# Kernel tuning notes

Measured on AMD Instinct MI355X. Metric: run time of the kernel, lower is better.

## Reference

```python
import jax, jax.numpy as jnp
import numpy as np

CONF_THRESH = 0.01
TOP_K = 200
NMS_THRESH = 0.45


def setup_inputs() -> dict:
    key = jax.random.key(0)
    k1, k2, k3, k4, k5 = jax.random.split(key, 5)
    B, N, C = 32, 8732, 21
    return {
        "loc_data": jax.random.normal(k1, (B, N, 4), jnp.float32),
        "conf_data": jax.random.normal(k2, (B, N, C), jnp.float32),
        "pose_data": jax.random.normal(k3, (B, N, 32), jnp.float32),
        "line_data": jax.random.normal(k4, (B, N, 3), jnp.float32),
        "dbox_list": jax.random.uniform(k5, (N, 4), jnp.float32),
    }


def decode(loc, dbox):
    # loc, dbox: [N,4]; variances 0.1 / 0.2 as in the torch decode()
    cxcy = dbox[:, :2] + loc[:, :2] * 0.1 * dbox[:, 2:]
    wh = dbox[:, 2:] * jnp.exp(loc[:, 2:] * 0.2)
    mins = cxcy - wh / 2.0
    maxs = mins + wh
    return jnp.concatenate([mins, maxs], axis=1)  # [N,4] xyxy


def nms_class(boxes, scores, poses, lines):
    """Greedy NMS for one (batch, class). boxes [N,4], scores [N] (softmax probs).
    Matches torch nm_suppression: candidates are the top_k by score above
    conf_thresh; suppress IoU > overlap; at most top_k kept."""
    s0 = jnp.where(scores > CONF_THRESH, scores, -jnp.inf)
    _, cand_idx = jax.lax.top_k(s0, TOP_K)  # descending-score candidate pool
    cb = boxes[cand_idx]                     # [K,4]
    cs = s0[cand_idx]                        # [K], -inf where below threshold
    x1, y1, x2, y2 = cb[:, 0], cb[:, 1], cb[:, 2], cb[:, 3]
    area = (x2 - x1) * (y2 - y1)
    K = TOP_K
    ar = jnp.arange(K)

    def step(s, _):
        i = jnp.argmax(s)
        take = jnp.isfinite(s[i])
        xx1 = jnp.maximum(x1, x1[i])
        yy1 = jnp.maximum(y1, y1[i])
        xx2 = jnp.minimum(x2, x2[i])
        yy2 = jnp.minimum(y2, y2[i])
        inter = jnp.clip(xx2 - xx1, 0.0) * jnp.clip(yy2 - yy1, 0.0)
        union = area - inter + area[i]
        iou = inter / union
        supp = (iou > NMS_THRESH) | (ar == i)
        s_new = jnp.where(take & supp, -jnp.inf, s)
        return s_new, (i, take)

    _, (pos, take) = jax.lax.scan(step, cs, None, length=K)
    gi = cand_idx[pos]  # global box indices of kept detections [K]
    row = jnp.concatenate(
        [scores[gi][:, None], boxes[gi], poses[gi], lines[gi]], axis=1
    )  # [K, 1+4+32+3] = [200, 40]
    return row * take[:, None].astype(row.dtype)


def reference(loc_data, conf_data, pose_data, line_data, dbox_list):
    conf = jax.nn.softmax(conf_data, axis=-1)                       # [B,N,C]
    boxes = jax.vmap(decode, in_axes=(0, None))(loc_data, dbox_list)  # [B,N,4]
    per_cls = jax.vmap(nms_class, in_axes=(None, 1, None, None))    # over classes
    per_batch = jax.vmap(per_cls, in_axes=(0, 0, 0, 0))             # over batch
    out = per_batch(boxes, conf, pose_data, line_data)              # [B,C,200,40]
    return out.at[:, 0].set(0.0)  # class 0 (background) is skipped in torch loop
```

## Files before the change

### kernel.cpp

```cpp
#include <hip/hip_runtime.h>
#include <math.h>

#define BB 32
#define NN 8732
#define CC 21
#define TOPK 200
#define NPOSE 32
#define NLINE 3
#define NBINS 2048
#define CAP 1024
#define ROWW 40

__device__ __forceinline__ double fexp(double x) {
  const double LOG2E = 1.4426950408889634074;
  const double LN2HI = 6.93147180369123816490e-01;
  const double LN2LO = 1.90821492927058770002e-10;
  double kd = rint(x * LOG2E);
  double r = fma(-kd, LN2HI, x);
  r = fma(-kd, LN2LO, r);
  double p = 2.08767569878680989792e-09;
  p = fma(p, r, 2.50521083854417187751e-08);
  p = fma(p, r, 2.75573192239858906526e-07);
  p = fma(p, r, 2.75573192239858925110e-06);
  p = fma(p, r, 2.48015873015873015873e-05);
  p = fma(p, r, 1.98412698412698412698e-04);
  p = fma(p, r, 1.38888888888888888889e-03);
  p = fma(p, r, 8.33333333333333333333e-03);
  p = fma(p, r, 4.16666666666666666667e-02);
  p = fma(p, r, 1.66666666666666666667e-01);
  p = fma(p, r, 0.5);
  p = fma(p, r, 1.0);
  p = fma(p, r, 1.0);
  int k = (int)kd;
  k = k < -1020 ? -1020 : (k > 1020 ? 1020 : k);
  double sc = __longlong_as_double((long long)(1023 + k) << 52);
  return p * sc;
}

__global__ __launch_bounds__(256, 4) void score_kernel(
    const float* __restrict__ conf, float* __restrict__ scores) {
  __shared__ __align__(16) float buf[256 * CC];
  const int tid = threadIdx.x;
  const int i0 = blockIdx.x * 256;
  const int base = i0 * CC;
  int total = BB * NN * CC - base;
  if (total > 256 * CC) total = 256 * CC;
  {
    const float4* g4 = (const float4*)(conf + base);
    float4* b4 = (float4*)buf;
    const int n4 = total >> 2;
    for (int t = tid; t < n4; t += 256) b4[t] = g4[t];
  }
  __syncthreads();
  const int i = i0 + tid;
  if (i >= BB * NN) return;
  const float* p = buf + tid * CC;
  float x[CC];
#pragma unroll
  for (int c = 0; c < CC; ++c) x[c] = p[c];
  float m = x[0];
#pragma unroll
  for (int c = 1; c < CC; ++c) m = fmaxf(m, x[c]);
  float e[CC];
#pragma unroll
  for (int c = 0; c < CC; ++c) e[c] = (float)fexp((double)(x[c] - m));
  float r0 = e[0] + e[8], r1 = e[1] + e[9], r2 = e[2] + e[10], r3 = e[3] + e[11];
  float r4 = e[4] + e[12], r5 = e[5] + e[13], r6 = e[6] + e[14], r7 = e[7] + e[15];
  float sum = ((r0 + r1) + (r2 + r3)) + ((r4 + r5) + (r6 + r7));
  sum += e[16]; sum += e[17]; sum += e[18]; sum += e[19]; sum += e[20];
  const int b = i / NN, n = i - b * NN;
#pragma unroll
  for (int c = 0; c < CC; ++c)
    scores[((size_t)b * CC + c) * NN + n] = e[c] / sum;
}

__device__ __forceinline__ int score_bin(float s) {
  unsigned u = __float_as_uint(s);
  int bin = (int)(u >> 15) - 30720;
  return bin < 0 ? 0 : (bin > NBINS - 1 ? NBINS - 1 : bin);
}

__device__ __forceinline__ float score_full(const float* conf, int b, int c, int n) {
  const float* p = conf + ((size_t)b * NN + n) * CC;
  float mm = p[0];
  for (int c2 = 1; c2 < CC; ++c2) mm = fmaxf(mm, p[c2]);
  float e[CC];
  for (int c2 = 0; c2 < CC; ++c2) e[c2] = (float)fexp((double)(p[c2] - mm));
  float r0 = e[0] + e[8], r1 = e[1] + e[9], r2 = e[2] + e[10], r3 = e[3] + e[11];
  float r4 = e[4] + e[12], r5 = e[5] + e[13], r6 = e[6] + e[14], r7 = e[7] + e[15];
  float sum = ((r0 + r1) + (r2 + r3)) + ((r4 + r5) + (r6 + r7));
  sum += e[16]; sum += e[17]; sum += e[18]; sum += e[19]; sum += e[20];
  return e[c] / sum;
}

__global__ __launch_bounds__(256) void nms_kernel(
    const float* __restrict__ loc, const float* __restrict__ conf,
    const float* __restrict__ pose, const float* __restrict__ line,
    const float* __restrict__ dbox, const float* __restrict__ scores,
    int mode, float* __restrict__ out) {
  const int bc = blockIdx.x;
  const int b = bc / CC, c = bc - b * CC;
  const int tid = threadIdx.x;
  const int wv = tid >> 6, lane = tid & 63;
  float* outSlab = out + (size_t)bc * (TOPK * ROWW);
  const float4 z4 = make_float4(0.f, 0.f, 0.f, 0.f);

  if (c == 0) {
    float4* o4 = (float4*)outSlab;
    for (int i = tid; i < TOPK * ROWW / 4; i += 256) o4[i] = z4;
    return;
  }

  __shared__ int hist[NBINS];
  __shared__ unsigned long long ckey[CAP];
  __shared__ float4 cbox[TOPK];
  __shared__ float carea[TOPK];
  __shared__ float sScore[TOPK];
  __shared__ int sIdx[TOPK];
  __shared__ unsigned long long supp[TOPK * 4];
  __shared__ unsigned long long rowAnyBits[4];
  __shared__ int kept[TOPK];
  __shared__ int waveTot[4];
  __shared__ int sBT, sCnt, sKept;

  for (int i = tid; i < NBINS; i += 256) hist[i] = 0;
  if (tid == 0) { sCnt = 0; sBT = 0; }
  __syncthreads();

  const float* scoresB = scores + ((size_t)b * CC + c) * NN;

  float4 v[9];
  if (mode == 1) {
#pragma unroll
    for (int k = 0; k < 8; ++k)
      v[k] = *(const float4*)(scoresB + k * 1024 + tid * 4);
    if (tid < 135)
      v[8] = *(const float4*)(scoresB + 8192 + tid * 4);
    else
      v[8] = make_float4(-1.f, -1.f, -1.f, -1.f);
  } else {
#pragma unroll 1
    for (int k = 0; k < 9; ++k) {
      const int n0 = k * 1024 + (tid << 2);
      if (k < 8 || tid < 135) {
        v[k].x = score_full(conf, b, c, n0 + 0);
        v[k].y = score_full(conf, b, c, n0 + 1);
        v[k].z = score_full(conf, b, c, n0 + 2);
        v[k].w = score_full(conf, b, c, n0 + 3);
      } else {
        v[k] = make_float4(-1.f, -1.f, -1.f, -1.f);
      }
    }
  }

#pragma unroll
  for (int k = 0; k < 9; ++k) {
    if (v[k].x > 0.01f) atomicAdd(&hist[score_bin(v[k].x)], 1);
    if (v[k].y > 0.01f) atomicAdd(&hist[score_bin(v[k].y)], 1);
    if (v[k].z > 0.01f) atomicAdd(&hist[score_bin(v[k].z)], 1);
    if (v[k].w > 0.01f) atomicAdd(&hist[score_bin(v[k].w)], 1);
  }
  __syncthreads();

  int s8 = 0;
#pragma unroll
  for (int k = 0; k < 8; ++k) s8 += hist[tid * 8 + k];
  int cs = s8;
#pragma unroll
  for (int d = 1; d < 64; d <<= 1) {
    int t = __shfl_down(cs, d, 64);
    if (lane + d < 64) cs += t;
  }
  if (lane == 0) waveTot[wv] = cs;
  __syncthreads();
  {
    int higher = 0;
    for (int g = wv + 1; g < 4; ++g) higher += waveTot[g];
    int incl = cs + higher;
    int excl = incl - s8;
    if (excl < TOPK && incl >= TOPK) {
      int cum = excl, bt = tid * 8;
      for (int bin = tid * 8 + 7;; --bin) {
        cum += hist[bin];
        if (cum >= TOPK || bin == tid * 8) { bt = bin; break; }
      }
      sBT = bt;
    }
  }
  __syncthreads();
  const int bt = sBT;

#pragma unroll
  for (int k = 0; k < 9; ++k) {
    float sv[4] = {v[k].x, v[k].y, v[k].z, v[k].w};
#pragma unroll
    for (int j = 0; j < 4; ++j) {
      float s = sv[j];
      if (s > 0.01f && score_bin(s) >= bt) {
        int p = atomicAdd(&sCnt, 1);
        if (p < CAP) {
          unsigned n = (unsigned)(k * 1024 + (tid << 2) + j);
          ckey[p] = ((unsigned long long)__float_as_uint(s) << 32) |
                    (unsigned long long)(0xFFFFFFFFu - n);
        }
      }
    }
  }
  __syncthreads();
  const int M = sCnt < CAP ? sCnt : CAP;
  if (M == 0) {
    float4* o4 = (float4*)outSlab;
    for (int i = tid; i < TOPK * ROWW / 4; i += 256) o4[i] = z4;
    return;
  }
  const int K = M < TOPK ? M : TOPK;

  for (int t = tid; t < M; t += 256) {
    unsigned long long kt = ckey[t];
    int r = 0;
    for (int j = 0; j < M; ++j) r += (ckey[j] > kt) ? 1 : 0;
    if (r < TOPK) {
      sScore[r] = __uint_as_float((unsigned)(kt >> 32));
      sIdx[r] = (int)(0xFFFFFFFFu - (unsigned)(kt & 0xFFFFFFFFull));
    }
  }
  __syncthreads();

  const float* locB = loc + (size_t)b * NN * 4;
  if (tid < K) {
    int n = sIdx[tid];
    float4 l4 = *(const float4*)(locB + (size_t)n * 4);
    float4 d4 = *(const float4*)(dbox + (size_t)n * 4);
    float cx = d4.x + (l4.x * 0.1f) * d4.z;
    float cy = d4.y + (l4.y * 0.1f) * d4.w;
    float w = d4.z * (float)fexp((double)(l4.z * 0.2f));
    float h = d4.w * (float)fexp((double)(l4.w * 0.2f));
    float x1 = cx - w * 0.5f;
    float y1 = cy - h * 0.5f;
    float x2 = x1 + w;
    float y2 = y1 + h;
    cbox[tid] = make_float4(x1, y1, x2, y2);
    carea[tid] = (x2 - x1) * (y2 - y1);
  }
  __syncthreads();

  {
    const double TMID = (double)0.45f + 0x1p-26;
    const int l = wv * 64 + lane;
    const bool lvalid = l < K;
    float4 lb = lvalid ? cbox[l] : z4;
    float lar = lvalid ? carea[l] : 0.f;
    const int jlim = (K < wv * 64 + 63) ? K : (wv * 64 + 63);
    for (int j = 0; j < jlim; ++j) {
      float4 jb = cbox[j];
      float ja = carea[j];
      float xx1 = fmaxf(lb.x, jb.x);
      float yy1 = fmaxf(lb.y, jb.y);
      float xx2 = fminf(lb.z, jb.z);
      float yy2 = fminf(lb.w, jb.w);
      float iw = fmaxf(xx2 - xx1, 0.0f);
      float ih = fmaxf(yy2 - yy1, 0.0f);
      float inter = iw * ih;
      float uni = (lar - inter) + ja;
      double tt = fma(-TMID, (double)uni, (double)inter);
      bool hit = lvalid & (l > j) & (tt > 0.0);
      unsigned long long mres = __ballot((int)hit);
      if (lane == 0) supp[j * 4 + wv] = mres;
    }
    if (lane == 0)
      for (int j = jlim; j < K; ++j) supp[j * 4 + wv] = 0ull;
  }
  __syncthreads();

  {
    bool nz = false;
    if (tid < K)
      nz = (supp[tid * 4 + 0] | supp[tid * 4 + 1] |
            supp[tid * 4 + 2] | supp[tid * 4 + 3]) != 0ull;
    unsigned long long bal = __ballot((int)nz);
    if (lane == 0) rowAnyBits[wv] = bal;
  }
  __syncthreads();

  if (tid == 0) {
    unsigned long long alive[4];
#pragma unroll
    for (int w = 0; w < 4; ++w) {
      int cnt = K - w * 64;
      alive[w] = cnt <= 0 ? 0ull : (cnt >= 64 ? ~0ull : ((1ull << cnt) - 1ull));
    }
    int nk = 0;
#pragma unroll
    for (int w = 0; w < 4; ++w) {
      const unsigned long long raw = rowAnyBits[w];
      while (alive[w]) {
        int bit = __ffsll(alive[w]) - 1;
        int j = w * 64 + bit;
        kept[nk++] = j;
        alive[w] &= ~(1ull << bit);
        if ((raw >> bit) & 1) {
          unsigned long long r0 = supp[j * 4 + 0];
          unsigned long long r1 = supp[j * 4 + 1];
          unsigned long long r2 = supp[j * 4 + 2];
          unsigned long long r3 = supp[j * 4 + 3];
          alive[0] &= ~r0; alive[1] &= ~r1; alive[2] &= ~r2; alive[3] &= ~r3;
        }
      }
    }
    sKept = nk;
  }
  __syncthreads();

  const int nk = sKept;
  const float* poseB = pose + (size_t)b * NN * NPOSE;
  const float* lineB = line + (size_t)b * NN * NLINE;
  for (int t = tid; t < nk; t += 256) {
    int j = kept[t];
    int n = sIdx[j];
    float* row = outSlab + (size_t)t * ROWW;
    float4 bx = cbox[j];
    row[0] = sScore[j];
    row[1] = bx.x;
    row[2] = bx.y;
    row[3] = bx.z;
    row[4] = bx.w;
    const float4* p4 = (const float4*)(poseB + (size_t)n * NPOSE);
#pragma unroll
    for (int q = 0; q < 8; ++q) {
      float4 pv = p4[q];
      row[5 + 4 * q + 0] = pv.x;
      row[5 + 4 * q + 1] = pv.y;
      row[5 + 4 * q + 2] = pv.z;
      row[5 + 4 * q + 3] = pv.w;
    }
    row[37] = lineB[(size_t)n * NLINE + 0];
    row[38] = lineB[(size_t)n * NLINE + 1];
    row[39] = lineB[(size_t)n * NLINE + 2];
  }
  {
    const int zq = (TOPK - nk) * 10;
    float4* o4 = (float4*)(outSlab + (size_t)nk * ROWW);
    for (int q = tid; q < zq; q += 256) o4[q] = z4;
  }
}

extern "C" void kernel_launch(void* const* d_in, const int* in_sizes, int n_in,
                              void* d_out, int out_size, void* d_ws, size_t ws_size,
                              hipStream_t stream) {
  const float* loc  = (const float*)d_in[0];
  const float* conf = (const float*)d_in[1];
  const float* pose = (const float*)d_in[2];
  const float* line = (const float*)d_in[3];
  const float* dbox = (const float*)d_in[4];
  float* out = (float*)d_out;

  const size_t scoreBytes = (size_t)BB * CC * NN * sizeof(float);
  int mode = (ws_size >= scoreBytes) ? 1 : 0;
  float* scores = mode ? (float*)d_ws : nullptr;

  if (mode) {
    const int total = BB * NN;
    score_kernel<<<(total + 255) / 256, 256, 0, stream>>>(conf, scores);
  }
  nms_kernel<<<BB * CC, 256, 0, stream>>>(loc, conf, pose, line, dbox,
                                          scores, mode, out);
}
```

Baseline: 194.1 us.

## Use table-based exp in softmax and unroll rank-sort and IoU loops

The softmax score kernel replaces a degree-12 double polynomial exp with a 64-entry shared-memory table plus a degree-4 polynomial, which cuts FP64 work per element. The candidate rank sort now reads keys in 16-wide vectorized chunks over a zero-padded array. The IoU suppression-matrix loop is unrolled by 8, batching LDS loads and ballots. The trade-offs are extra shared memory, extra registers, and a small accuracy difference in the exp approximation.

```diff
diff --git a/kernel.cpp b/kernel.cpp
--- a/kernel.cpp
+++ b/kernel.cpp
@@ -11,7 +11,7 @@
 #define CAP 1024
 #define ROWW 40
 
-__device__ __forceinline__ double fexp(double x) {
+__device__ __forceinline__ double fexp12(double x) {
   const double LOG2E = 1.4426950408889634074;
   const double LN2HI = 6.93147180369123816490e-01;
   const double LN2LO = 1.90821492927058770002e-10;
@@ -37,9 +37,30 @@
   return p * sc;
 }
 
+__device__ __forceinline__ double fexp_t(double x, const double* __restrict__ T) {
+  const double INV64 = 1.4426950408889634074 * 64.0;
+  const double L64HI = 6.93147180369123816490e-01 / 64.0;
+  const double L64LO = 1.90821492927058770002e-10 / 64.0;
+  double kd = rint(x * INV64);
+  double r = fma(-kd, L64HI, x);
+  r = fma(-kd, L64LO, r);
+  double p = 4.16666666666666666667e-02;
+  p = fma(p, r, 1.66666666666666666667e-01);
+  p = fma(p, r, 0.5);
+  p = fma(p, r, 1.0);
+  p = fma(p, r, 1.0);
+  int ki = (int)kd;
+  double t = T[ki & 63];
+  int e = ki >> 6;
+  e = e < -1020 ? -1020 : e;
+  double sc = __longlong_as_double((long long)(1023 + e) << 52);
+  return (t * p) * sc;
+}
+
 __global__ __launch_bounds__(256, 4) void score_kernel(
     const float* __restrict__ conf, float* __restrict__ scores) {
   __shared__ __align__(16) float buf[256 * CC];
+  __shared__ double Texp[64];
   const int tid = threadIdx.x;
   const int i0 = blockIdx.x * 256;
   const int base = i0 * CC;
@@ -51,6 +72,8 @@
     const int n4 = total >> 2;
     for (int t = tid; t < n4; t += 256) b4[t] = g4[t];
   }
+  if (tid < 64)
+    Texp[tid] = fexp12((double)tid * (6.93147180369123816490e-01 / 64.0));
   __syncthreads();
   const int i = i0 + tid;
   if (i >= BB * NN) return;
@@ -63,7 +86,7 @@
   for (int c = 1; c < CC; ++c) m = fmaxf(m, x[c]);
   float e[CC];
 #pragma unroll
-  for (int c = 0; c < CC; ++c) e[c] = (float)fexp((double)(x[c] - m));
+  for (int c = 0; c < CC; ++c) e[c] = (float)fexp_t((double)(x[c] - m), Texp);
   float r0 = e[0] + e[8], r1 = e[1] + e[9], r2 = e[2] + e[10], r3 = e[3] + e[11];
   float r4 = e[4] + e[12], r5 = e[5] + e[13], r6 = e[6] + e[14], r7 = e[7] + e[15];
   float sum = ((r0 + r1) + (r2 + r3)) + ((r4 + r5) + (r6 + r7));
@@ -85,7 +108,7 @@
   float mm = p[0];
   for (int c2 = 1; c2 < CC; ++c2) mm = fmaxf(mm, p[c2]);
   float e[CC];
-  for (int c2 = 0; c2 < CC; ++c2) e[c2] = (float)fexp((double)(p[c2] - mm));
+  for (int c2 = 0; c2 < CC; ++c2) e[c2] = (float)fexp12((double)(p[c2] - mm));
   float r0 = e[0] + e[8], r1 = e[1] + e[9], r2 = e[2] + e[10], r3 = e[3] + e[11];
   float r4 = e[4] + e[12], r5 = e[5] + e[13], r6 = e[6] + e[14], r7 = e[7] + e[15];
   float sum = ((r0 + r1) + (r2 + r3)) + ((r4 + r5) + (r6 + r7));
@@ -112,7 +135,7 @@
   }
 
   __shared__ int hist[NBINS];
-  __shared__ unsigned long long ckey[CAP];
+  __shared__ __align__(16) unsigned long long ckey[CAP + 16];
   __shared__ float4 cbox[TOPK];
   __shared__ float carea[TOPK];
   __shared__ float sScore[TOPK];
@@ -214,11 +237,24 @@
     return;
   }
   const int K = M < TOPK ? M : TOPK;
+  const int Mpad = (M + 15) & ~15;
+  for (int i = M + tid; i < Mpad; i += 256) ckey[i] = 0ull;
+  __syncthreads();
 
   for (int t = tid; t < M; t += 256) {
     unsigned long long kt = ckey[t];
     int r = 0;
-    for (int j = 0; j < M; ++j) r += (ckey[j] > kt) ? 1 : 0;
+    for (int j0 = 0; j0 < Mpad; j0 += 16) {
+      ulonglong2 kk[8];
+#pragma unroll
+      for (int q = 0; q < 8; ++q)
+        kk[q] = *(const ulonglong2*)(ckey + j0 + 2 * q);
+#pragma unroll
+      for (int q = 0; q < 8; ++q) {
+        r += (kk[q].x > kt) ? 1 : 0;
+        r += (kk[q].y > kt) ? 1 : 0;
+      }
+    }
     if (r < TOPK) {
       sScore[r] = __uint_as_float((unsigned)(kt >> 32));
       sIdx[r] = (int)(0xFFFFFFFFu - (unsigned)(kt & 0xFFFFFFFFull));
@@ -233,8 +269,8 @@
     float4 d4 = *(const float4*)(dbox + (size_t)n * 4);
     float cx = d4.x + (l4.x * 0.1f) * d4.z;
     float cy = d4.y + (l4.y * 0.1f) * d4.w;
-    float w = d4.z * (float)fexp((double)(l4.z * 0.2f));
-    float h = d4.w * (float)fexp((double)(l4.w * 0.2f));
+    float w = d4.z * (float)fexp12((double)(l4.z * 0.2f));
+    float h = d4.w * (float)fexp12((double)(l4.w * 0.2f));
     float x1 = cx - w * 0.5f;
     float y1 = cy - h * 0.5f;
     float x2 = x1 + w;
@@ -251,21 +287,35 @@
     float4 lb = lvalid ? cbox[l] : z4;
     float lar = lvalid ? carea[l] : 0.f;
     const int jlim = (K < wv * 64 + 63) ? K : (wv * 64 + 63);
-    for (int j = 0; j < jlim; ++j) {
-      float4 jb = cbox[j];
-      float ja = carea[j];
-      float xx1 = fmaxf(lb.x, jb.x);
-      float yy1 = fmaxf(lb.y, jb.y);
-      float xx2 = fminf(lb.z, jb.z);
-      float yy2 = fminf(lb.w, jb.w);
-      float iw = fmaxf(xx2 - xx1, 0.0f);
-      float ih = fmaxf(yy2 - yy1, 0.0f);
-      float inter = iw * ih;
-      float uni = (lar - inter) + ja;
-      double tt = fma(-TMID, (double)uni, (double)inter);
-      bool hit = lvalid & (l > j) & (tt > 0.0);
-      unsigned long long mres = __ballot((int)hit);
-      if (lane == 0) supp[j * 4 + wv] = mres;
+    for (int j0 = 0; j0 < jlim; j0 += 8) {
+      const int jc = (jlim - j0 < 8) ? (jlim - j0) : 8;
+      float4 jb[8];
+      float ja[8];
+#pragma unroll
+      for (int q = 0; q < 8; ++q)
+        if (q < jc) { jb[q] = cbox[j0 + q]; ja[q] = carea[j0 + q]; }
+      unsigned long long mres[8];
+#pragma unroll
+      for (int q = 0; q < 8; ++q) {
+        if (q < jc) {
+          float xx1 = fmaxf(lb.x, jb[q].x);
+          float yy1 = fmaxf(lb.y, jb[q].y);
+          float xx2 = fminf(lb.z, jb[q].z);
+          float yy2 = fminf(lb.w, jb[q].w);
+          float iw = fmaxf(xx2 - xx1, 0.0f);
+          float ih = fmaxf(yy2 - yy1, 0.0f);
+          float inter = iw * ih;
+          float uni = (lar - inter) + ja[q];
+          double tt = fma(-TMID, (double)uni, (double)inter);
+          bool hit = lvalid & (l > (j0 + q)) & (tt > 0.0);
+          mres[q] = __ballot((int)hit);
+        }
+      }
+      if (lane == 0) {
+#pragma unroll
+        for (int q = 0; q < 8; ++q)
+          if (q < jc) supp[(j0 + q) * 4 + wv] = mres[q];
+      }
     }
     if (lane == 0)
       for (int j = jlim; j < K; ++j) supp[j * 4 + wv] = 0ull;
```

Measured after the change: 192.0 us. About the same (-1.1%).
